# Kernel optimization log

Hardware: AMD Instinct MI355X
Metric: run time of the kernel (lower is better)

Reference implementation:

```python
import jax, jax.numpy as jnp
import numpy as np
import math

N, T, D, H = 64, 512, 1024, 1024

def setup_inputs() -> dict:
    key = jax.random.key(0)
    k1, k2, k3, k4 = jax.random.split(key, 4)
    x = jax.random.normal(k1, (N, T, D), dtype=jnp.float32)
    h0 = jax.random.normal(k2, (N, H), dtype=jnp.float32)
    Wx = jax.random.normal(k3, (D, 4 * H), dtype=jnp.float32) / math.sqrt(D)
    Wh = jax.random.normal(k4, (H, 4 * H), dtype=jnp.float32) / math.sqrt(H)
    b = jnp.zeros((4 * H,), dtype=jnp.float32)
    return {"x": x, "h0": h0, "Wx": Wx, "Wh": Wh, "b": b}

def lstm_forward(x, h0, Wx, Wh, b):
    Hd = h0.shape[1]
    # Precompute input-to-hidden contribution for all timesteps in one GEMM.
    xW = jnp.einsum('ntd,dg->ntg', x, Wx) + b  # (N, T, 4H)
    c0 = jnp.zeros_like(h0)

    def step(carry, xw_t):
        prev_h, prev_c = carry
        a = xw_t + prev_h @ Wh  # (N, 4H)
        i = jax.nn.sigmoid(a[:, :Hd])
        f = jax.nn.sigmoid(a[:, Hd:2 * Hd])
        o = jax.nn.sigmoid(a[:, 2 * Hd:3 * Hd])
        g = jnp.tanh(a[:, 3 * Hd:])
        next_c = f * prev_c + i * g
        next_h = o * jnp.tanh(next_c)
        return (next_h, next_c), next_h

    # scan over time axis: move T to leading dim
    (_, _), hs = jax.lax.scan(step, (h0, c0), jnp.swapaxes(xW, 0, 1))
    return jnp.swapaxes(hs, 0, 1)  # (N, T, H)

def reference(x, h0, Wx, Wh, b):
    return lstm_forward(x, h0, Wx, Wh, b)
```

## Files before the change

### kernel.cpp

```cpp
#include <hip/hip_runtime.h>


#define NB 64
#define TT 512
#define DD 1024
#define HH 1024
#define GG 4096
#define FSTRIDE 32

using f32x4  = __attribute__((ext_vector_type(4))) float;
using bf16x8 = __attribute__((ext_vector_type(8))) __bf16;
using u16x4  = __attribute__((ext_vector_type(4))) unsigned short;

__device__ inline unsigned short f2bf(float x) {
  union { float f; unsigned u; } v; v.f = x;
  unsigned r = v.u + 0x7fffu + ((v.u >> 16) & 1u);
  return (unsigned short)(r >> 16);
}
__device__ inline float bfu2f(unsigned short u) {
  union { unsigned u; float f; } v; v.u = ((unsigned)u) << 16; return v.f;
}
__device__ inline float sigm(float x)     { return 1.0f / (1.0f + __expf(-x)); }
__device__ inline float tanhfast(float x) { return 1.0f - 2.0f / (__expf(2.0f * x) + 1.0f); }

__global__ __launch_bounds__(256) void tcast(const float* __restrict__ in,
                                             unsigned short* __restrict__ out,
                                             int rows, int cols) {
  __shared__ float tile[32][33];
  const int bx = blockIdx.x * 32;
  const int by = blockIdx.y * 32;
  const int tx = threadIdx.x;
  for (int i = threadIdx.y; i < 32; i += 8)
    tile[i][tx] = in[(size_t)(by + i) * cols + bx + tx];
  __syncthreads();
  for (int i = threadIdx.y; i < 32; i += 8)
    out[(size_t)(bx + i) * rows + by + tx] = f2bf(tile[tx][i]);
}

__global__ __launch_bounds__(256) void init_h(const float* __restrict__ h0,
                                              unsigned* __restrict__ hp,
                                              int* __restrict__ bar) {
  const int idx = blockIdx.x * 256 + threadIdx.x;
  const float v = h0[idx];
  const unsigned short hi = f2bf(v);
  const unsigned short lo = f2bf(v - bfu2f(hi));
  hp[idx] = ((unsigned)hi << 16) | lo;
  if (blockIdx.x == 0)
    for (int i = threadIdx.x; i < 256 * FSTRIDE; i += 256) bar[i] = 0;
}

#define BM 128
#define BN 128
#define BK 64
#define LDP (BK + 8)

__global__ __launch_bounds__(256) void gemm_xw(const float* __restrict__ x,
                                               const unsigned short* __restrict__ WxT,
                                               const float* __restrict__ bvec,
                                               unsigned short* __restrict__ xw) {
  __shared__ unsigned short As[BM][LDP];
  __shared__ unsigned short Bs[BN][LDP];
  const int tid  = threadIdx.x;
  const int m0   = blockIdx.y * BM;
  const int g0   = blockIdx.x * BN;
  const int wave = tid >> 6, lane = tid & 63;
  const int wm = (wave & 1) * 64, wn = (wave >> 1) * 64;
  const int lr = lane & 15, lk = (lane >> 4) * 8;

  f32x4 acc[4][4] = {};

  for (int kt = 0; kt < DD; kt += BK) {
#pragma unroll
    for (int it = 0; it < 8; ++it) {
      const int row = it * 16 + (tid >> 4);
      const int c4  = (tid & 15) * 4;
      const float4 xv = *(const float4*)(x + (size_t)(m0 + row) * DD + kt + c4);
      u16x4 us; us.x = f2bf(xv.x); us.y = f2bf(xv.y); us.z = f2bf(xv.z); us.w = f2bf(xv.w);
      *(u16x4*)&As[row][c4] = us;
    }
#pragma unroll
    for (int it = 0; it < 4; ++it) {
      const int row = it * 32 + (tid >> 3);
      const int c8  = (tid & 7) * 8;
      const uint4 wv = *(const uint4*)(WxT + (size_t)(g0 + row) * DD + kt + c8);
      *(uint4*)&Bs[row][c8] = wv;
    }
    __syncthreads();
#pragma unroll
    for (int ks = 0; ks < BK / 32; ++ks) {
      const int kk = ks * 32 + lk;
      bf16x8 af[4], bfv[4];
#pragma unroll
      for (int mi = 0; mi < 4; ++mi) af[mi]  = *(const bf16x8*)&As[wm + mi * 16 + lr][kk];
#pragma unroll
      for (int ni = 0; ni < 4; ++ni) bfv[ni] = *(const bf16x8*)&Bs[wn + ni * 16 + lr][kk];
#pragma unroll
      for (int mi = 0; mi < 4; ++mi)
#pragma unroll
        for (int ni = 0; ni < 4; ++ni)
          acc[mi][ni] = __builtin_amdgcn_mfma_f32_16x16x32_bf16(af[mi], bfv[ni], acc[mi][ni], 0, 0, 0);
    }
    __syncthreads();
  }

#pragma unroll
  for (int mi = 0; mi < 4; ++mi) {
    const int row = m0 + wm + mi * 16 + ((lane >> 4) << 2);
#pragma unroll
    for (int ni = 0; ni < 4; ++ni) {
      const int col = g0 + wn + ni * 16 + lr;
      const float bb = bvec[col];
#pragma unroll
      for (int j = 0; j < 4; ++j)
        xw[(size_t)(row + j) * GG + col] = f2bf(acc[mi][ni][j] + bb);
    }
  }
}

__global__ __launch_bounds__(512, 1) void lstm_seq(
    const unsigned short* __restrict__ WhT,
    const unsigned short* __restrict__ xw,
    unsigned* __restrict__ hp0, unsigned* __restrict__ hp1,
    float* __restrict__ out, int* __restrict__ bar) {
  __shared__ unsigned short As_hi[16][1024];
  __shared__ unsigned short As_lo[16][1024];
  __shared__ float abuf[4][16][34];

  const int tid  = threadIdx.x;
  const int bid  = blockIdx.x;
  const int grp  = bid & 3;
  const int qid  = bid >> 2;
  const int r0   = grp * 16;
  const int j0   = qid * 32;
  const int w    = tid >> 6;
  const int gate = w & 3;
  const int ch   = w >> 2;
  const int lane = tid & 63;
  const int lr   = lane & 15;
  const int kslot = lane >> 4;
  const int sx   = lr & 7;
  const int srow = tid >> 5;
  const int swr  = srow & 7;
  const int re   = tid >> 5, ce = tid & 31;

  int* myflag = &bar[(grp * 32 + qid) * FSTRIDE];

  bf16x8 rB[32];
  {
    const unsigned short* wrow =
        WhT + ((size_t)(gate * HH + j0 + ch * 16 + lr)) * HH + kslot * 8;
#pragma unroll
    for (int ks = 0; ks < 32; ++ks)
      rB[ks] = *(const bf16x8*)&wrow[ks * 32];
  }

  float creg = 0.0f;

  const size_t xrc = (size_t)(r0 + re) * TT * GG + j0 + ce;
  unsigned short xc0 = xw[xrc + 0 * HH];
  unsigned short xc1 = xw[xrc + 1 * HH];
  unsigned short xc2 = xw[xrc + 2 * HH];
  unsigned short xc3 = xw[xrc + 3 * HH];

  for (int t = 0; t < TT; ++t) {
    unsigned* hp = (t & 1) ? hp1 : hp0;
    unsigned* np = (t & 1) ? hp0 : hp1;

    const unsigned* hrow = hp + (size_t)(r0 + srow) * HH;
    const int c0 = 0 * 32 + (tid & 31), c1 = 1 * 32 + (tid & 31);
    const int c2 = 2 * 32 + (tid & 31), c3 = 3 * 32 + (tid & 31);
    const unsigned* p0 = hrow + c0 * 8;
    const unsigned* p1 = hrow + c1 * 8;
    const unsigned* p2 = hrow + c2 * 8;
    const unsigned* p3 = hrow + c3 * 8;
    uint4 q0, q1, q2, q3, q4, q5, q6, q7;
    asm volatile(
        "global_load_dwordx4 %0, %[a0], off sc0 sc1\n\t"
        "global_load_dwordx4 %1, %[a0], off offset:16 sc0 sc1\n\t"
        "global_load_dwordx4 %2, %[a1], off sc0 sc1\n\t"
        "global_load_dwordx4 %3, %[a1], off offset:16 sc0 sc1\n\t"
        "global_load_dwordx4 %4, %[a2], off sc0 sc1\n\t"
        "global_load_dwordx4 %5, %[a2], off offset:16 sc0 sc1\n\t"
        "global_load_dwordx4 %6, %[a3], off sc0 sc1\n\t"
        "global_load_dwordx4 %7, %[a3], off offset:16 sc0 sc1\n\t"
        "s_waitcnt vmcnt(0)"
        : "=&v"(q0), "=&v"(q1), "=&v"(q2), "=&v"(q3),
          "=&v"(q4), "=&v"(q5), "=&v"(q6), "=&v"(q7)
        : [a0] "v"(p0), [a1] "v"(p1), [a2] "v"(p2), [a3] "v"(p3)
        : "memory");

#define UNPACK(QA, QB, CC)                                                    \
    {                                                                         \
      const int sc = (CC) ^ swr;                                              \
      uint4 HI, LO;                                                           \
      HI.x = (QA.x >> 16) | (QA.y & 0xffff0000u);                             \
      HI.y = (QA.z >> 16) | (QA.w & 0xffff0000u);                             \
      HI.z = (QB.x >> 16) | (QB.y & 0xffff0000u);                             \
      HI.w = (QB.z >> 16) | (QB.w & 0xffff0000u);                             \
      LO.x = (QA.x & 0xffffu) | (QA.y << 16);                                 \
      LO.y = (QA.z & 0xffffu) | (QA.w << 16);                                 \
      LO.z = (QB.x & 0xffffu) | (QB.y << 16);                                 \
      LO.w = (QB.z & 0xffffu) | (QB.w << 16);                                 \
      *(uint4*)&As_hi[srow][sc * 8] = HI;                                     \
      *(uint4*)&As_lo[srow][sc * 8] = LO;                                     \
    }
    UNPACK(q0, q1, c0) UNPACK(q2, q3, c1) UNPACK(q4, q5, c2) UNPACK(q6, q7, c3)
#undef UNPACK
    __syncthreads();

    const int tn = (t + 1 < TT) ? t + 1 : t;
    const size_t xa = xrc + (size_t)tn * GG;
    const unsigned short nx0 = xw[xa + 0 * HH];
    const unsigned short nx1 = xw[xa + 1 * HH];
    const unsigned short nx2 = xw[xa + 2 * HH];
    const unsigned short nx3 = xw[xa + 3 * HH];

    f32x4 aHE = {}, aHO = {}, aLE = {}, aLO = {};
#pragma unroll
    for (int ks = 0; ks < 32; ks += 2) {
      const int cc0 = ((ks)     * 4 + kslot) ^ sx;
      const int cc1 = ((ks + 1) * 4 + kslot) ^ sx;
      const bf16x8 ah0 = *(const bf16x8*)&As_hi[lr][cc0 * 8];
      const bf16x8 al0 = *(const bf16x8*)&As_lo[lr][cc0 * 8];
      const bf16x8 ah1 = *(const bf16x8*)&As_hi[lr][cc1 * 8];
      const bf16x8 al1 = *(const bf16x8*)&As_lo[lr][cc1 * 8];
      aHE = __builtin_amdgcn_mfma_f32_16x16x32_bf16(ah0, rB[ks],     aHE, 0, 0, 0);
      aLE = __builtin_amdgcn_mfma_f32_16x16x32_bf16(al0, rB[ks],     aLE, 0, 0, 0);
      aHO = __builtin_amdgcn_mfma_f32_16x16x32_bf16(ah1, rB[ks + 1], aHO, 0, 0, 0);
      aLO = __builtin_amdgcn_mfma_f32_16x16x32_bf16(al1, rB[ks + 1], aLO, 0, 0, 0);
    }
    const f32x4 accv = (aHE + aHO) + (aLE + aLO);

#pragma unroll
    for (int j = 0; j < 4; ++j)
      abuf[gate][(lane >> 4) * 4 + j][ch * 16 + lr] = accv[j];
    __syncthreads();

    const float ai = abuf[0][re][ce] + bfu2f(xc0);
    const float af = abuf[1][re][ce] + bfu2f(xc1);
    const float ao = abuf[2][re][ce] + bfu2f(xc2);
    const float ag = abuf[3][re][ce] + bfu2f(xc3);

    const float gi = sigm(ai), gf = sigm(af), go = sigm(ao), gg = tanhfast(ag);
    creg = gf * creg + gi * gg;
    const float hn = go * tanhfast(creg);

    out[((size_t)(r0 + re) * TT + t) * HH + j0 + ce] = hn;
    const unsigned short hi = f2bf(hn);
    const unsigned pack = ((unsigned)hi << 16) | f2bf(hn - bfu2f(hi));
    __hip_atomic_store(&np[(size_t)(r0 + re) * HH + j0 + ce], pack,
                       __ATOMIC_RELAXED, __HIP_MEMORY_SCOPE_AGENT);

    xc0 = nx0; xc1 = nx1; xc2 = nx2; xc3 = nx3;

    if (t + 1 < TT) {
      asm volatile("s_waitcnt vmcnt(0)" ::: "memory");
      __syncthreads();
      if (tid == 0)
        __hip_atomic_store(myflag, t + 1, __ATOMIC_RELAXED, __HIP_MEMORY_SCOPE_AGENT);
      if (tid < 32) {
        while (__hip_atomic_load(&bar[(grp * 32 + tid) * FSTRIDE],
                                 __ATOMIC_RELAXED, __HIP_MEMORY_SCOPE_AGENT) < t + 1) {}
      }
      __builtin_amdgcn_sched_barrier(0);
      __syncthreads();
    }
  }
}

extern "C" void kernel_launch(void* const* d_in, const int* in_sizes, int n_in,
                              void* d_out, int out_size, void* d_ws, size_t ws_size,
                              hipStream_t stream) {
  const float* x  = (const float*)d_in[0];
  const float* h0 = (const float*)d_in[1];
  const float* Wx = (const float*)d_in[2];
  const float* Wh = (const float*)d_in[3];
  const float* b  = (const float*)d_in[4];
  float* out = (float*)d_out;

  unsigned short* xw  = (unsigned short*)d_ws;
  unsigned short* WxT = xw  + (size_t)NB * TT * GG;
  unsigned short* WhT = WxT + (size_t)GG * DD;
  unsigned* hp0 = (unsigned*)(WhT + (size_t)GG * HH);
  unsigned* hp1 = hp0 + (size_t)NB * HH;
  int* bar = (int*)(hp1 + (size_t)NB * HH);

  tcast<<<dim3(GG / 32, DD / 32), dim3(32, 8), 0, stream>>>(Wx, WxT, DD, GG);
  tcast<<<dim3(GG / 32, HH / 32), dim3(32, 8), 0, stream>>>(Wh, WhT, HH, GG);
  init_h<<<NB * HH / 256, 256, 0, stream>>>(h0, hp0, bar);
  gemm_xw<<<dim3(GG / BN, NB * TT / BM), 256, 0, stream>>>(x, WxT, b, xw);

  lstm_seq<<<128, 512, 0, stream>>>(WhT, xw, hp0, hp1, out, bar);
}
```

Baseline: 3.267 ms.

## Replace flag-based inter-block barrier with parity tags embedded in h data

Removes the per-step flag array and its global spin barrier. Each step instead writes a parity tag into the low bit of the bf16 low-part of every packed h value. Consumers poll the h buffer directly until all loaded words carry the expected tag, which removes one global round-trip and two block-wide syncs per timestep. In exchange, one bit of the low-order correction term is lost, and every consumer thread re-reads its full h slice while it spins, which adds memory traffic.

Measured after the change: 4.050 ms. 24.0% more time.

```diff
diff --git a/kernel.cpp b/kernel.cpp
--- a/kernel.cpp
+++ b/kernel.cpp
@@ -6,7 +6,6 @@
 #define DD 1024
 #define HH 1024
 #define GG 4096
-#define FSTRIDE 32
 
 using f32x4  = __attribute__((ext_vector_type(4))) float;
 using bf16x8 = __attribute__((ext_vector_type(8))) __bf16;
@@ -38,15 +37,14 @@
 }
 
 __global__ __launch_bounds__(256) void init_h(const float* __restrict__ h0,
-                                              unsigned* __restrict__ hp,
-                                              int* __restrict__ bar) {
+                                              unsigned* __restrict__ hp0,
+                                              unsigned* __restrict__ hp1) {
   const int idx = blockIdx.x * 256 + threadIdx.x;
   const float v = h0[idx];
   const unsigned short hi = f2bf(v);
   const unsigned short lo = f2bf(v - bfu2f(hi));
-  hp[idx] = ((unsigned)hi << 16) | lo;
-  if (blockIdx.x == 0)
-    for (int i = threadIdx.x; i < 256 * FSTRIDE; i += 256) bar[i] = 0;
+  hp0[idx] = ((unsigned)hi << 16) | ((unsigned)(lo & 0xFFFEu));
+  hp1[idx] = 1u;
 }
 
 #define BM 128
@@ -121,7 +119,7 @@
     const unsigned short* __restrict__ WhT,
     const unsigned short* __restrict__ xw,
     unsigned* __restrict__ hp0, unsigned* __restrict__ hp1,
-    float* __restrict__ out, int* __restrict__ bar) {
+    float* __restrict__ out) {
   __shared__ unsigned short As_hi[16][1024];
   __shared__ unsigned short As_lo[16][1024];
   __shared__ float abuf[4][16][34];
@@ -143,8 +141,6 @@
   const int swr  = srow & 7;
   const int re   = tid >> 5, ce = tid & 31;
 
-  int* myflag = &bar[(grp * 32 + qid) * FSTRIDE];
-
   bf16x8 rB[32];
   {
     const unsigned short* wrow =
@@ -173,21 +169,34 @@
     const unsigned* p1 = hrow + c1 * 8;
     const unsigned* p2 = hrow + c2 * 8;
     const unsigned* p3 = hrow + c3 * 8;
+    const unsigned expect = (unsigned)((t >> 1) & 1);
     uint4 q0, q1, q2, q3, q4, q5, q6, q7;
-    asm volatile(
-        "global_load_dwordx4 %0, %[a0], off sc0 sc1\n\t"
-        "global_load_dwordx4 %1, %[a0], off offset:16 sc0 sc1\n\t"
-        "global_load_dwordx4 %2, %[a1], off sc0 sc1\n\t"
-        "global_load_dwordx4 %3, %[a1], off offset:16 sc0 sc1\n\t"
-        "global_load_dwordx4 %4, %[a2], off sc0 sc1\n\t"
-        "global_load_dwordx4 %5, %[a2], off offset:16 sc0 sc1\n\t"
-        "global_load_dwordx4 %6, %[a3], off sc0 sc1\n\t"
-        "global_load_dwordx4 %7, %[a3], off offset:16 sc0 sc1\n\t"
-        "s_waitcnt vmcnt(0)"
-        : "=&v"(q0), "=&v"(q1), "=&v"(q2), "=&v"(q3),
-          "=&v"(q4), "=&v"(q5), "=&v"(q6), "=&v"(q7)
-        : [a0] "v"(p0), [a1] "v"(p1), [a2] "v"(p2), [a3] "v"(p3)
-        : "memory");
+    for (;;) {
+      asm volatile(
+          "global_load_dwordx4 %0, %[a0], off sc0 sc1\n\t"
+          "global_load_dwordx4 %1, %[a0], off offset:16 sc0 sc1\n\t"
+          "global_load_dwordx4 %2, %[a1], off sc0 sc1\n\t"
+          "global_load_dwordx4 %3, %[a1], off offset:16 sc0 sc1\n\t"
+          "global_load_dwordx4 %4, %[a2], off sc0 sc1\n\t"
+          "global_load_dwordx4 %5, %[a2], off offset:16 sc0 sc1\n\t"
+          "global_load_dwordx4 %6, %[a3], off sc0 sc1\n\t"
+          "global_load_dwordx4 %7, %[a3], off offset:16 sc0 sc1\n\t"
+          "s_waitcnt vmcnt(0)"
+          : "=&v"(q0), "=&v"(q1), "=&v"(q2), "=&v"(q3),
+            "=&v"(q4), "=&v"(q5), "=&v"(q6), "=&v"(q7)
+          : [a0] "v"(p0), [a1] "v"(p1), [a2] "v"(p2), [a3] "v"(p3)
+          : "memory");
+      const unsigned av = q0.x & q0.y & q0.z & q0.w & q1.x & q1.y & q1.z & q1.w &
+                          q2.x & q2.y & q2.z & q2.w & q3.x & q3.y & q3.z & q3.w &
+                          q4.x & q4.y & q4.z & q4.w & q5.x & q5.y & q5.z & q5.w &
+                          q6.x & q6.y & q6.z & q6.w & q7.x & q7.y & q7.z & q7.w;
+      const unsigned ov = q0.x | q0.y | q0.z | q0.w | q1.x | q1.y | q1.z | q1.w |
+                          q2.x | q2.y | q2.z | q2.w | q3.x | q3.y | q3.z | q3.w |
+                          q4.x | q4.y | q4.z | q4.w | q5.x | q5.y | q5.z | q5.w |
+                          q6.x | q6.y | q6.z | q6.w | q7.x | q7.y | q7.z | q7.w;
+      const unsigned chk = expect ? av : ~ov;
+      if (chk & 1u) break;
+    }
 
 #define UNPACK(QA, QB, CC)                                                    \
     {                                                                         \
@@ -247,24 +256,13 @@
 
     out[((size_t)(r0 + re) * TT + t) * HH + j0 + ce] = hn;
     const unsigned short hi = f2bf(hn);
-    const unsigned pack = ((unsigned)hi << 16) | f2bf(hn - bfu2f(hi));
+    const unsigned short lo = f2bf(hn - bfu2f(hi));
+    const unsigned tag = (unsigned)(((t + 1) >> 1) & 1);
+    const unsigned pack = ((unsigned)hi << 16) | ((unsigned)(lo & 0xFFFEu) | tag);
     __hip_atomic_store(&np[(size_t)(r0 + re) * HH + j0 + ce], pack,
                        __ATOMIC_RELAXED, __HIP_MEMORY_SCOPE_AGENT);
 
     xc0 = nx0; xc1 = nx1; xc2 = nx2; xc3 = nx3;
-
-    if (t + 1 < TT) {
-      asm volatile("s_waitcnt vmcnt(0)" ::: "memory");
-      __syncthreads();
-      if (tid == 0)
-        __hip_atomic_store(myflag, t + 1, __ATOMIC_RELAXED, __HIP_MEMORY_SCOPE_AGENT);
-      if (tid < 32) {
-        while (__hip_atomic_load(&bar[(grp * 32 + tid) * FSTRIDE],
-                                 __ATOMIC_RELAXED, __HIP_MEMORY_SCOPE_AGENT) < t + 1) {}
-      }
-      __builtin_amdgcn_sched_barrier(0);
-      __syncthreads();
-    }
   }
 }
 
@@ -283,12 +281,11 @@
   unsigned short* WhT = WxT + (size_t)GG * DD;
   unsigned* hp0 = (unsigned*)(WhT + (size_t)GG * HH);
   unsigned* hp1 = hp0 + (size_t)NB * HH;
-  int* bar = (int*)(hp1 + (size_t)NB * HH);
 
   tcast<<<dim3(GG / 32, DD / 32), dim3(32, 8), 0, stream>>>(Wx, WxT, DD, GG);
   tcast<<<dim3(GG / 32, HH / 32), dim3(32, 8), 0, stream>>>(Wh, WhT, HH, GG);
-  init_h<<<NB * HH / 256, 256, 0, stream>>>(h0, hp0, bar);
+  init_h<<<NB * HH / 256, 256, 0, stream>>>(h0, hp0, hp1);
   gemm_xw<<<dim3(GG / BN, NB * TT / BM), 256, 0, stream>>>(x, WxT, b, xw);
 
-  lstm_seq<<<128, 512, 0, stream>>>(WhT, xw, hp0, hp1, out, bar);
-}
+  lstm_seq<<<128, 512, 0, stream>>>(WhT, xw, hp0, hp1, out);
+}
```
